# Performance work log

Measured on AMD Instinct MI355X. Metric: run time of the kernel, lower is better.

Reference implementation:

```python
import jax, jax.numpy as jnp
import numpy as np

E, K, H, I, GS, T, C = 64, 4, 2048, 1536, 128, 1024, 128

# FP4 E2M1 lookup table: sign bit in nibble MSB, magnitudes {0,.5,1,1.5,2,3,4,6}
LUT = jnp.array([0.0, 0.5, 1.0, 1.5, 2.0, 3.0, 4.0, 6.0,
                 -0.0, -0.5, -1.0, -1.5, -2.0, -3.0, -4.0, -6.0], dtype=jnp.float32)


def _dequant(packed, scales):
    """packed: [O, I//8] int32 (8 FP4 nibbles/word), scales: [I//GS, O] -> W [O, I] fp32."""
    O, IW = packed.shape
    shifts = (jnp.arange(8, dtype=jnp.int32) * 4)
    nib = (packed[:, :, None] >> shifts) & 0xF          # [O, IW, 8]
    vals = LUT[nib].reshape(O, IW * 8)                   # [O, I]
    g = jnp.arange(IW * 8) // GS                         # group index per input col
    return vals * scales.T[:, g]                         # [O, I]


def _mlp(x2d, gp, gs, up, us, dp, ds):
    """SwiGLU expert: down( silu(x Wg^T) * (x Wu^T) )."""
    Wg = _dequant(gp, gs)
    Wu = _dequant(up, us)
    Wd = _dequant(dp, ds)
    h = jax.nn.silu(x2d @ Wg.T) * (x2d @ Wu.T)           # [N, I]
    return h @ Wd.T                                      # [N, H]


def setup_inputs() -> dict:
    key = jax.random.key(0)
    ks = jax.random.split(key, 16)
    ri = lambda k, sh: jax.random.randint(k, sh, 0, 2**31 - 1, dtype=jnp.int32)
    sc = lambda k, sh: jax.random.uniform(k, sh, dtype=jnp.float32) * 0.02 + 0.001
    return {
        "x": jax.random.normal(ks[0], (T, H), dtype=jnp.float32),
        "gate_w": jax.random.normal(ks[1], (E, H), dtype=jnp.float32) * 0.02,
        "gate_scales": sc(ks[2], (E, H // GS, I)),
        "up_scales": sc(ks[3], (E, H // GS, I)),
        "down_scales": sc(ks[4], (E, I // GS, H)),
        "sh_gate_scales": sc(ks[5], (H // GS, I)),
        "sh_up_scales": sc(ks[6], (H // GS, I)),
        "sh_down_scales": sc(ks[7], (I // GS, H)),
        "gate_packed": ri(ks[8], (E, I, H // 8)),
        "up_packed": ri(ks[9], (E, I, H // 8)),
        "down_packed": ri(ks[10], (E, H, I // 8)),
        "sh_gate_packed": ri(ks[11], (I, H // 8)),
        "sh_up_packed": ri(ks[12], (I, H // 8)),
        "sh_down_packed": ri(ks[13], (H, I // 8)),
    }


def reference(x, gate_w, gate_scales, up_scales, down_scales,
              sh_gate_scales, sh_up_scales, sh_down_scales,
              gate_packed, up_packed, down_packed,
              sh_gate_packed, sh_up_packed, sh_down_packed):
    # --- top-k routing ---
    probs = jax.nn.softmax(x @ gate_w.T, axis=-1)        # [T, E]
    tw, ti = jax.lax.top_k(probs, K)                     # [T, K]
    tw = tw / tw.sum(-1, keepdims=True)
    # --- dispatch with fixed capacity C per expert ---
    A = T * K
    ef = ti.reshape(-1)                                  # [A] expert id per assignment
    tok = jnp.arange(A) // K                             # source token per assignment
    counts = jax.ops.segment_sum(jnp.ones(A, jnp.int32), ef, num_segments=E)
    starts = jnp.cumsum(counts) - counts                 # [E]
    sidx = jnp.argsort(ef)
    pos_sorted = jnp.arange(A, dtype=jnp.int32) - starts[ef[sidx]]
    pos = jnp.zeros(A, jnp.int32).at[sidx].set(pos_sorted)  # rank within expert
    slot = ef * C + pos
    valid = pos < C
    buf = jnp.zeros((E * C + 1, H), x.dtype).at[jnp.where(valid, slot, E * C)].set(x[tok])
    buf = buf[:E * C].reshape(E, C, H)
    # --- per-expert fused dequant + SwiGLU (scan over experts) ---
    def body(_, xs):
        b, gp, gs, up, us, dp, ds = xs
        return None, _mlp(b, gp, gs, up, us, dp, ds)
    _, eout = jax.lax.scan(body, None,
                           (buf, gate_packed, gate_scales, up_packed, up_scales,
                            down_packed, down_scales))
    # --- combine ---
    rows = eout.reshape(E * C, H)
    gath = rows[jnp.where(valid, slot, 0)] * valid[:, None].astype(x.dtype)
    y = (gath.reshape(T, K, H) * tw[..., None]).sum(axis=1)
    # --- shared expert ---
    y = y + _mlp(x, sh_gate_packed, sh_gate_scales, sh_up_packed, sh_up_scales,
                 sh_down_packed, sh_down_scales)
    return y
```

## Files before the change

kernel.cpp:

```cpp
#include <hip/hip_runtime.h>
#include <stdint.h>

#define E_ 64
#define KTOP 4
#define H_ 2048
#define I_ 1536
#define GS_ 128
#define T_ 1024
#define CAP 128

typedef __attribute__((ext_vector_type(8))) short short8;
typedef __attribute__((ext_vector_type(4))) float f32x4;

__device__ __forceinline__ uint32_t bf16rne(float f) {
  uint32_t u = __float_as_uint(f);
  return (u + 0x7FFFu + ((u >> 16) & 1u)) >> 16;
}
__device__ __forceinline__ float bf16f(uint32_t b) {
  return __uint_as_float(b << 16);
}

__global__ void cast_x_kernel(const float* __restrict__ x, uint16_t* __restrict__ xb, int n4) {
  int i = blockIdx.x * blockDim.x + threadIdx.x;
  if (i >= n4) return;
  float4 v = ((const float4*)x)[i];
  uint32_t lo = bf16rne(v.x) | (bf16rne(v.y) << 16);
  uint32_t hi = bf16rne(v.z) | (bf16rne(v.w) << 16);
  uint2 r; r.x = lo; r.y = hi;
  ((uint2*)xb)[i] = r;
}

__global__ void transpose_gw_kernel(const float* __restrict__ gw, float* __restrict__ gwT) {
  int o = blockIdx.x * 256 + threadIdx.x;
  int k = o >> 6, e = o & 63;
  gwT[o] = gw[(long)e * H_ + k];
}

__global__ __launch_bounds__(256) void routing_kernel(
    const float* __restrict__ x, const float* __restrict__ gwT,
    float* __restrict__ tw, int* __restrict__ ti) {
  int t = blockIdx.x;
  int tid = threadIdx.x;
  __shared__ float xs[H_];
  __shared__ float lgp[4][E_];
  const float4* xp = (const float4*)(x + (long)t * H_);
  ((float4*)xs)[tid] = xp[tid];
  ((float4*)xs)[tid + 256] = xp[tid + 256];
  __syncthreads();
  int e = tid & 63, w4 = tid >> 6;
  const float* gp = gwT + (long)w4 * 512 * E_ + e;
  const float* xw = xs + w4 * 512;
  float a0 = 0.f, a1 = 0.f, a2 = 0.f, a3 = 0.f;
#pragma unroll 4
  for (int k = 0; k < 512; k += 4) {
    a0 += xw[k]     * gp[(long)(k)     * E_];
    a1 += xw[k + 1] * gp[(long)(k + 1) * E_];
    a2 += xw[k + 2] * gp[(long)(k + 2) * E_];
    a3 += xw[k + 3] * gp[(long)(k + 3) * E_];
  }
  lgp[w4][e] = (a0 + a1) + (a2 + a3);
  __syncthreads();
  if (tid < 64) {
    int lane = tid;
    float v = lgp[0][lane] + lgp[1][lane] + lgp[2][lane] + lgp[3][lane];
    float vals[KTOP]; int ids[KTOP];
#pragma unroll
    for (int k = 0; k < KTOP; k++) {
      float bv = v; int bi = lane;
      for (int off = 32; off; off >>= 1) {
        float ov = __shfl_xor(bv, off);
        int oi = __shfl_xor(bi, off);
        if (ov > bv || (ov == bv && oi < bi)) { bv = ov; bi = oi; }
      }
      vals[k] = bv; ids[k] = bi;
      if (lane == bi) v = -3.4e38f;
    }
    if (lane == 0) {
      float m = vals[0];
      float p[KTOP]; float s = 0.f;
#pragma unroll
      for (int k = 0; k < KTOP; k++) { p[k] = expf(vals[k] - m); s += p[k]; }
      float inv = 1.f / s;
#pragma unroll
      for (int k = 0; k < KTOP; k++) {
        tw[t * KTOP + k] = p[k] * inv;
        ti[t * KTOP + k] = ids[k];
      }
    }
  }
}

__global__ void assign_kernel(const int* __restrict__ ti, int* __restrict__ counts,
                              int* __restrict__ tlist, int* __restrict__ slot_of) {
  int e = blockIdx.x;
  int lane = threadIdx.x;
  int cnt = 0;
  for (int base = 0; base < T_ * KTOP; base += 64) {
    int a = base + lane;
    int ef = ti[a];
    unsigned long long m = __ballot(ef == e);
    if (ef == e) {
      int rank = cnt + __popcll(m & ((1ull << lane) - 1ull));
      if (rank < CAP) {
        tlist[e * CAP + rank] = a >> 2;
        slot_of[a] = e * CAP + rank;
      } else {
        slot_of[a] = -1;
      }
    }
    cnt += __popcll(m);
  }
  if (lane == 0) counts[e] = min(cnt, CAP);
}

__global__ __launch_bounds__(256, 3) void gemm_fp4_kernel(
    const uint16_t* __restrict__ A1, const uint16_t* __restrict__ A2, int ldA,
    const int* __restrict__ rowids, const int* __restrict__ counts, int nE,
    const int* __restrict__ packed1, long p_stride,
    const float* __restrict__ scales1, long s_stride,
    const int* __restrict__ packed2, const float* __restrict__ scales2,
    void* __restrict__ out1, int of1, void* __restrict__ out2, int of2,
    int K, int N) {
  __shared__ uint16_t As[2][128 * 64];
  __shared__ uint16_t Bs[8 * 128 * 8];

  int yb = blockIdx.y, bn = blockIdx.x;
  int tid = threadIdx.x;
  int wave = tid >> 6, lane = tid & 63;

  const uint16_t* A;
  const int* packed_e;
  const float* scales_e;
  char* outp;
  int of32, row_base, valid;
  const int* rid = nullptr;
  if (yb < nE) {
    int e = yb;
    valid = counts[e];
    if (valid <= 0) return;
    if (valid > 128) valid = 128;
    if (rowids) rid = rowids + e * CAP;
    row_base = e * CAP;
    A = A1;
    packed_e = packed1 + (long)e * p_stride;
    scales_e = scales1 + (long)e * s_stride;
    outp = (char*)out1; of32 = of1;
  } else {
    valid = 128;
    row_base = (yb - nE) * 128;
    A = A2;
    packed_e = packed2;
    scales_e = scales2;
    outp = (char*)out2; of32 = of2;
  }

  const uint16_t* asrc[4];
  int adst[4];
#pragma unroll
  for (int ii = 0; ii < 4; ii++) {
    int inst = wave * 4 + ii;
    int r = inst * 8 + (lane >> 3);
    int rr = r < valid ? r : valid - 1;
    long arow = rid ? (long)rid[rr] : (long)(row_base + rr);
    int g = (lane & 7) ^ (r & 7);
    asrc[ii] = A + arow * (long)ldA + (g << 3);
    adst[ii] = inst * 512;
  }

  int j = tid >> 1, wseg = tid & 1;
  int n_col = bn * 128 + j;
  const int* prow = packed_e + (long)n_col * (K >> 3) + wseg * 4;
  uint16_t* bdst = Bs + ((long)(wseg * 4) * 128 + j) * 8;

  f32x4 acc[4][4];
#pragma unroll
  for (int a0 = 0; a0 < 4; a0++)
#pragma unroll
    for (int b0 = 0; b0 < 4; b0++) {
      f32x4 z = {0.f, 0.f, 0.f, 0.f};
      acc[a0][b0] = z;
    }

  int wm = wave >> 1, wn = wave & 1;
  int q = lane >> 4, r16 = lane & 15;

  int nk = K >> 6;

  uint4 bpk_c = *(const uint4*)prow;
  float scl_c = scales_e[n_col];
#pragma unroll
  for (int ii = 0; ii < 4; ii++)
    __builtin_amdgcn_global_load_lds(
        (const __attribute__((address_space(1))) unsigned int*)asrc[ii],
        (__attribute__((address_space(3))) unsigned int*)(&As[0][0] + adst[ii]),
        16, 0, 0);
  uint4 bpk_n = bpk_c;
  float scl_n = scl_c;

  for (int it = 0; it < nk; ++it) {
    int b = it & 1;
    int kt2 = (it + 1) << 6;
    int pf = (it + 1 < nk);
    if (pf) {
      bpk_n = *(const uint4*)(prow + (kt2 >> 3));
      scl_n = scales_e[(long)(kt2 >> 7) * N + n_col];
      uint16_t* ab = &As[b ^ 1][0];
#pragma unroll
      for (int ii = 0; ii < 4; ii++)
        __builtin_amdgcn_global_load_lds(
            (const __attribute__((address_space(1))) unsigned int*)(asrc[ii] + kt2),
            (__attribute__((address_space(3))) unsigned int*)(ab + adst[ii]),
            16, 0, 0);
    }
    {
      float s = scl_c;
      uint32_t b1 = bf16rne(s), b15 = bf16rne(1.5f * s);
      uint32_t t0 = 0, t1 = b1 - 0x80, t2 = b1, t3 = b15;
      uint32_t t4 = b1 + 0x80, t5 = b15 + 0x80, t6 = b1 + 0x100, t7 = b15 + 0x100;
      uint32_t tll = (t0 & 0xFF) | ((t1 & 0xFF) << 8) | ((t2 & 0xFF) << 16) | ((t3 & 0xFF) << 24);
      uint32_t tlh = (t4 & 0xFF) | ((t5 & 0xFF) << 8) | ((t6 & 0xFF) << 16) | ((t7 & 0xFF) << 24);
      uint32_t thl = (t0 >> 8) | ((t1 >> 8) << 8) | ((t2 >> 8) << 16) | ((t3 >> 8) << 24);
      uint32_t thh = (t4 >> 8) | ((t5 >> 8) << 8) | ((t6 >> 8) << 16) | ((t7 >> 8) << 24);
      uint32_t wsv[4] = {bpk_c.x, bpk_c.y, bpk_c.z, bpk_c.w};
#pragma unroll
      for (int w = 0; w < 4; w++) {
        uint32_t wv = wsv[w];
        uint32_t ev = wv & 0x07070707u;
        uint32_t od = (wv >> 4) & 0x07070707u;
        uint32_t se = (wv << 4) & 0x80808080u;
        uint32_t so = wv & 0x80808080u;
        uint32_t he = __builtin_amdgcn_perm(thh, thl, ev) | se;
        uint32_t ho = __builtin_amdgcn_perm(thh, thl, od) | so;
        uint32_t le = __builtin_amdgcn_perm(tlh, tll, ev);
        uint32_t lo = __builtin_amdgcn_perm(tlh, tll, od);
        uint32_t v02 = __builtin_amdgcn_perm(he, le, 0x05010400u);
        uint32_t v46 = __builtin_amdgcn_perm(he, le, 0x07030602u);
        uint32_t v13 = __builtin_amdgcn_perm(ho, lo, 0x05010400u);
        uint32_t v57 = __builtin_amdgcn_perm(ho, lo, 0x07030602u);
        uint4 qv;
        qv.x = __builtin_amdgcn_perm(v13, v02, 0x05040100u);
        qv.y = __builtin_amdgcn_perm(v13, v02, 0x07060302u);
        qv.z = __builtin_amdgcn_perm(v57, v46, 0x05040100u);
        qv.w = __builtin_amdgcn_perm(v57, v46, 0x07060302u);
        *(uint4*)(bdst + (long)w * 1024) = qv;
      }
    }
    if (pf) asm volatile("s_waitcnt vmcnt(6) lgkmcnt(0)" ::: "memory");
    else    asm volatile("s_waitcnt vmcnt(0) lgkmcnt(0)" ::: "memory");
    __builtin_amdgcn_sched_barrier(0);
    __builtin_amdgcn_s_barrier();
    __builtin_amdgcn_sched_barrier(0);

    const uint16_t* asb = &As[b][0];
    __builtin_amdgcn_s_setprio(1);
#pragma unroll
    for (int kk = 0; kk < 64; kk += 32) {
      int kc4 = (kk >> 3) + q;
      short8 af[4], bfr[4];
#pragma unroll
      for (int fm = 0; fm < 4; fm++) {
        int m = wm * 64 + fm * 16 + r16;
        af[fm] = *(const short8*)(asb + (long)m * 64 + ((kc4 ^ (m & 7)) << 3));
      }
#pragma unroll
      for (int fn = 0; fn < 4; fn++) {
        int n = wn * 64 + fn * 16 + r16;
        bfr[fn] = *(const short8*)(Bs + ((long)kc4 * 128 + n) * 8);
      }
#pragma unroll
      for (int fm = 0; fm < 4; fm++)
#pragma unroll
        for (int fn = 0; fn < 4; fn++)
          acc[fm][fn] = __builtin_amdgcn_mfma_f32_16x16x32_bf16(af[fm], bfr[fn], acc[fm][fn], 0, 0, 0);
    }
    __builtin_amdgcn_s_setprio(0);
    __builtin_amdgcn_sched_barrier(0);
    __builtin_amdgcn_s_barrier();
    __builtin_amdgcn_sched_barrier(0);
    bpk_c = bpk_n;
    scl_c = scl_n;
  }

  int outr0 = wm * 64 + (q << 2);
  int outc0 = bn * 128 + wn * 64 + r16;
#pragma unroll
  for (int fm = 0; fm < 4; fm++)
#pragma unroll
    for (int fn = 0; fn < 4; fn++) {
#pragma unroll
      for (int r = 0; r < 4; r++) {
        int rloc = outr0 + fm * 16 + r;
        if (rloc >= valid) continue;
        long row = row_base + rloc;
        long col = outc0 + fn * 16;
        float vv = acc[fm][fn][r];
        if (of32) ((float*)outp)[row * N + col] = vv;
        else ((uint16_t*)outp)[row * N + col] = (uint16_t)bf16rne(vv);
      }
    }
}

__global__ void silu_mul_kernel(const uint16_t* __restrict__ g, const uint16_t* __restrict__ u,
                                uint16_t* __restrict__ h, int n8) {
  int i = blockIdx.x * blockDim.x + threadIdx.x;
  if (i >= n8) return;
  uint4 gv = ((const uint4*)g)[i];
  uint4 uv = ((const uint4*)u)[i];
  uint32_t gw[4] = {gv.x, gv.y, gv.z, gv.w};
  uint32_t uw[4] = {uv.x, uv.y, uv.z, uv.w};
  uint32_t rw[4];
#pragma unroll
  for (int w = 0; w < 4; w++) {
    float g0 = bf16f(gw[w] & 0xFFFFu), g1 = bf16f(gw[w] >> 16);
    float u0 = bf16f(uw[w] & 0xFFFFu), u1 = bf16f(uw[w] >> 16);
    float r0 = g0 / (1.f + __expf(-g0)) * u0;
    float r1 = g1 / (1.f + __expf(-g1)) * u1;
    rw[w] = bf16rne(r0) | (bf16rne(r1) << 16);
  }
  uint4 res; res.x = rw[0]; res.y = rw[1]; res.z = rw[2]; res.w = rw[3];
  ((uint4*)h)[i] = res;
}

__global__ __launch_bounds__(256) void combine_kernel(
    float* __restrict__ y, const uint16_t* __restrict__ eout,
    const int* __restrict__ slot_of, const float* __restrict__ tw) {
  int t = blockIdx.x;
  int c = threadIdx.x * 8;
  float* yp = y + (long)t * H_ + c;
  float4 y0 = ((float4*)yp)[0];
  float4 y1 = ((float4*)yp)[1];
  float a[8] = {y0.x, y0.y, y0.z, y0.w, y1.x, y1.y, y1.z, y1.w};
#pragma unroll
  for (int k = 0; k < KTOP; k++) {
    int s = slot_of[t * KTOP + k];
    float w = tw[t * KTOP + k];
    if (s < 0) continue;
    uint4 v = *(const uint4*)(eout + (long)s * H_ + c);
    uint32_t vw[4] = {v.x, v.y, v.z, v.w};
#pragma unroll
    for (int jj = 0; jj < 4; jj++) {
      a[2 * jj]     += w * bf16f(vw[jj] & 0xFFFFu);
      a[2 * jj + 1] += w * bf16f(vw[jj] >> 16);
    }
  }
  float4 o0 = {a[0], a[1], a[2], a[3]};
  float4 o1 = {a[4], a[5], a[6], a[7]};
  ((float4*)yp)[0] = o0;
  ((float4*)yp)[1] = o1;
}

extern "C" void kernel_launch(void* const* d_in, const int* in_sizes, int n_in,
                              void* d_out, int out_size, void* d_ws, size_t ws_size,
                              hipStream_t stream) {
  const float* x              = (const float*)d_in[0];
  const float* gate_w         = (const float*)d_in[1];
  const float* gate_scales    = (const float*)d_in[2];
  const float* up_scales      = (const float*)d_in[3];
  const float* down_scales    = (const float*)d_in[4];
  const float* sh_gate_scales = (const float*)d_in[5];
  const float* sh_up_scales   = (const float*)d_in[6];
  const float* sh_down_scales = (const float*)d_in[7];
  const int* gate_packed      = (const int*)d_in[8];
  const int* up_packed        = (const int*)d_in[9];
  const int* down_packed      = (const int*)d_in[10];
  const int* sh_gate_packed   = (const int*)d_in[11];
  const int* sh_up_packed     = (const int*)d_in[12];
  const int* sh_down_packed   = (const int*)d_in[13];
  float* y = (float*)d_out;

  char* ws = (char*)d_ws;
  uint16_t* xb     = (uint16_t*)(ws);
  float*    tw     = (float*)(ws + 4194304);
  int*      ti     = (int*)(ws + 4210688);
  int*      counts = (int*)(ws + 4227072);
  int*      tlist  = (int*)(ws + 4227328);
  int*      slot_of= (int*)(ws + 4260096);
  uint16_t* gbuf   = (uint16_t*)(ws + 4276480);
  float*    gwT    = (float*)(ws + 4276480);
  uint16_t* ubuf   = (uint16_t*)(ws + 29442304);
  uint16_t* eout   = (uint16_t*)(ws + 29442304);
  uint16_t* gsbuf  = (uint16_t*)(ws + 62996736);
  uint16_t* usbuf  = (uint16_t*)(ws + 66142464);

  cast_x_kernel<<<2048, 256, 0, stream>>>(x, xb, T_ * H_ / 4);
  transpose_gw_kernel<<<512, 256, 0, stream>>>(gate_w, gwT);
  routing_kernel<<<T_, 256, 0, stream>>>(x, gwT, tw, ti);
  assign_kernel<<<E_, 64, 0, stream>>>(ti, counts, tlist, slot_of);

  gemm_fp4_kernel<<<dim3(12, 72, 1), 256, 0, stream>>>(
      xb, xb, H_, tlist, counts, E_,
      gate_packed, (long)I_ * (H_ / 8), gate_scales, (long)(H_ / GS_) * I_,
      sh_gate_packed, sh_gate_scales,
      gbuf, 0, gsbuf, 0, H_, I_);
  gemm_fp4_kernel<<<dim3(12, 72, 1), 256, 0, stream>>>(
      xb, xb, H_, tlist, counts, E_,
      up_packed, (long)I_ * (H_ / 8), up_scales, (long)(H_ / GS_) * I_,
      sh_up_packed, sh_up_scales,
      ubuf, 0, usbuf, 0, H_, I_);

  silu_mul_kernel<<<(E_ * CAP * I_ / 8 + 255) / 256, 256, 0, stream>>>(
      gbuf, ubuf, gbuf, E_ * CAP * I_ / 8);
  silu_mul_kernel<<<(T_ * I_ / 8 + 255) / 256, 256, 0, stream>>>(
      gsbuf, usbuf, gsbuf, T_ * I_ / 8);

  gemm_fp4_kernel<<<dim3(16, 72, 1), 256, 0, stream>>>(
      gbuf, gsbuf, I_, nullptr, counts, E_,
      down_packed, (long)H_ * (I_ / 8), down_scales, (long)(I_ / GS_) * H_,
      sh_down_packed, sh_down_scales,
      eout, 0, y, 1, I_, H_);

  combine_kernel<<<T_, 256, 0, stream>>>(y, eout, slot_of, tw);
}
```

Before: 546.1 us.

## Switch to fp16 register-side dequant, merge gate/up GEMMs and fuse small kernels

Activations and intermediates move from bf16 to fp16. FP4 weights are now dequantized straight into MFMA B-fragments in registers with a packed fp16 multiply by the scale, so the LDS B staging buffer and its barrier traffic go away. The x input is pre-permuted so the nibble order lines up, and the gate output columns are permuted back on write. Gate and up GEMMs run in one launch via grid z, the two silu launches are merged, and the cast and transpose kernels are fused into one. The trade-off is fp16 range and precision risk, plus redundant dequant work across the waves that share a column.

```diff
diff --git a/kernel.cpp b/kernel.cpp
--- a/kernel.cpp
+++ b/kernel.cpp
@@ -1,4 +1,5 @@
 #include <hip/hip_runtime.h>
+#include <hip/hip_fp16.h>
 #include <stdint.h>
 
 #define E_ 64
@@ -9,31 +10,57 @@
 #define T_ 1024
 #define CAP 128
 
-typedef __attribute__((ext_vector_type(8))) short short8;
-typedef __attribute__((ext_vector_type(4))) float f32x4;
-
-__device__ __forceinline__ uint32_t bf16rne(float f) {
-  uint32_t u = __float_as_uint(f);
-  return (u + 0x7FFFu + ((u >> 16) & 1u)) >> 16;
-}
-__device__ __forceinline__ float bf16f(uint32_t b) {
-  return __uint_as_float(b << 16);
-}
-
-__global__ void cast_x_kernel(const float* __restrict__ x, uint16_t* __restrict__ xb, int n4) {
-  int i = blockIdx.x * blockDim.x + threadIdx.x;
-  if (i >= n4) return;
-  float4 v = ((const float4*)x)[i];
-  uint32_t lo = bf16rne(v.x) | (bf16rne(v.y) << 16);
-  uint32_t hi = bf16rne(v.z) | (bf16rne(v.w) << 16);
-  uint2 r; r.x = lo; r.y = hi;
-  ((uint2*)xb)[i] = r;
-}
-
-__global__ void transpose_gw_kernel(const float* __restrict__ gw, float* __restrict__ gwT) {
-  int o = blockIdx.x * 256 + threadIdx.x;
-  int k = o >> 6, e = o & 63;
-  gwT[o] = gw[(long)e * H_ + k];
+typedef _Float16 f16x8 __attribute__((ext_vector_type(8)));
+typedef float f32x4 __attribute__((ext_vector_type(4)));
+
+__device__ __forceinline__ uint32_t f16pk(float a, float b) {
+  __half2 h = __floats2half2_rn(a, b);
+  return __builtin_bit_cast(uint32_t, h);
+}
+__device__ __forceinline__ uint32_t h2pk(float s) {
+  uint32_t u = (uint32_t)__builtin_bit_cast(uint16_t, __float2half(s));
+  return u | (u << 16);
+}
+__device__ __forceinline__ uint32_t pkmul(uint32_t a, uint32_t b) {
+  __half2 x = __builtin_bit_cast(__half2, a);
+  __half2 y = __builtin_bit_cast(__half2, b);
+  __half2 r = __hmul2(x, y);
+  return __builtin_bit_cast(uint32_t, r);
+}
+
+__device__ __forceinline__ f16x8 dq_f16(uint32_t w, uint32_t spk) {
+  uint32_t ev = w & 0x07070707u;
+  uint32_t od = (w >> 4) & 0x07070707u;
+  uint32_t se = (w << 4) & 0x80808080u;
+  uint32_t so = w & 0x80808080u;
+  uint32_t he = __builtin_amdgcn_perm(0x46444240u, 0x3E3C3800u, ev) | se;
+  uint32_t ho = __builtin_amdgcn_perm(0x46444240u, 0x3E3C3800u, od) | so;
+  uint4 r;
+  r.x = pkmul(__builtin_amdgcn_perm(he, 0u, 0x05000400u), spk);
+  r.y = pkmul(__builtin_amdgcn_perm(he, 0u, 0x07000600u), spk);
+  r.z = pkmul(__builtin_amdgcn_perm(ho, 0u, 0x05000400u), spk);
+  r.w = pkmul(__builtin_amdgcn_perm(ho, 0u, 0x07000600u), spk);
+  return __builtin_bit_cast(f16x8, r);
+}
+
+__global__ void prep_kernel(const float* __restrict__ x, uint16_t* __restrict__ xb,
+                            const float* __restrict__ gw, float* __restrict__ gwT) {
+  int b = blockIdx.x;
+  if (b < T_ * H_ / 8 / 256) {
+    int i = b * 256 + threadIdx.x;
+    const float4* xp = (const float4*)x;
+    float4 v0 = xp[2 * i], v1 = xp[2 * i + 1];
+    uint4 o;
+    o.x = f16pk(v0.x, v0.z);
+    o.y = f16pk(v1.x, v1.z);
+    o.z = f16pk(v0.y, v0.w);
+    o.w = f16pk(v1.y, v1.w);
+    ((uint4*)xb)[i] = o;
+  } else {
+    int o = (b - T_ * H_ / 8 / 256) * 256 + threadIdx.x;
+    int k = o >> 6, e = o & 63;
+    gwT[o] = gw[(long)e * H_ + k];
+  }
 }
 
 __global__ __launch_bounds__(256) void routing_kernel(
@@ -116,21 +143,22 @@
 __global__ __launch_bounds__(256, 3) void gemm_fp4_kernel(
     const uint16_t* __restrict__ A1, const uint16_t* __restrict__ A2, int ldA,
     const int* __restrict__ rowids, const int* __restrict__ counts, int nE,
-    const int* __restrict__ packed1, long p_stride,
-    const float* __restrict__ scales1, long s_stride,
-    const int* __restrict__ packed2, const float* __restrict__ scales2,
-    void* __restrict__ out1, int of1, void* __restrict__ out2, int of2,
-    int K, int N) {
+    const int* __restrict__ pk_e0, const int* __restrict__ pk_e1,
+    const float* __restrict__ sc_e0, const float* __restrict__ sc_e1,
+    long p_stride, long s_stride,
+    const int* __restrict__ pk_s0, const int* __restrict__ pk_s1,
+    const float* __restrict__ sc_s0, const float* __restrict__ sc_s1,
+    void* __restrict__ out_e0, void* __restrict__ out_e1,
+    void* __restrict__ out_s0, void* __restrict__ out_s1,
+    int K, int N, int of32_e, int of32_s, int perm_out) {
   __shared__ uint16_t As[2][128 * 64];
-  __shared__ uint16_t Bs[8 * 128 * 8];
-
-  int yb = blockIdx.y, bn = blockIdx.x;
-  int tid = threadIdx.x;
-  int wave = tid >> 6, lane = tid & 63;
+
+  int bn = blockIdx.x, yb = blockIdx.y, zs = blockIdx.z;
+  int tid = threadIdx.x, wave = tid >> 6, lane = tid & 63;
 
   const uint16_t* A;
-  const int* packed_e;
-  const float* scales_e;
+  const int* pk;
+  const float* sc;
   char* outp;
   int of32, row_base, valid;
   const int* rid = nullptr;
@@ -142,35 +170,43 @@
     if (rowids) rid = rowids + e * CAP;
     row_base = e * CAP;
     A = A1;
-    packed_e = packed1 + (long)e * p_stride;
-    scales_e = scales1 + (long)e * s_stride;
-    outp = (char*)out1; of32 = of1;
+    pk = (zs ? pk_e1 : pk_e0) + (long)e * p_stride;
+    sc = (zs ? sc_e1 : sc_e0) + (long)e * s_stride;
+    outp = (char*)(zs ? out_e1 : out_e0);
+    of32 = of32_e;
   } else {
     valid = 128;
     row_base = (yb - nE) * 128;
     A = A2;
-    packed_e = packed2;
-    scales_e = scales2;
-    outp = (char*)out2; of32 = of2;
-  }
-
-  const uint16_t* asrc[4];
-  int adst[4];
+    pk = zs ? pk_s1 : pk_s0;
+    sc = zs ? sc_s1 : sc_s0;
+    outp = (char*)(zs ? out_s1 : out_s0);
+    of32 = of32_s;
+  }
+
+  uint32_t a_off[4];
+  int lds_dst[4];
 #pragma unroll
   for (int ii = 0; ii < 4; ii++) {
     int inst = wave * 4 + ii;
     int r = inst * 8 + (lane >> 3);
     int rr = r < valid ? r : valid - 1;
-    long arow = rid ? (long)rid[rr] : (long)(row_base + rr);
-    int g = (lane & 7) ^ (r & 7);
-    asrc[ii] = A + arow * (long)ldA + (g << 3);
-    adst[ii] = inst * 512;
-  }
-
-  int j = tid >> 1, wseg = tid & 1;
-  int n_col = bn * 128 + j;
-  const int* prow = packed_e + (long)n_col * (K >> 3) + wseg * 4;
-  uint16_t* bdst = Bs + ((long)(wseg * 4) * 128 + j) * 8;
+    int arow = rid ? rid[rr] : row_base + rr;
+    a_off[ii] = (uint32_t)arow * (uint32_t)ldA + (uint32_t)((((lane & 7) ^ (r & 7)) << 3));
+    lds_dst[ii] = inst * 512;
+  }
+
+  int wm = wave >> 1, wn = wave & 1;
+  int q = lane >> 4, r16 = lane & 15;
+  int KW = K >> 3;
+
+  uint32_t bw_off[4], sc_off[4];
+#pragma unroll
+  for (int fn = 0; fn < 4; fn++) {
+    int c = bn * 128 + wn * 64 + fn * 16 + r16;
+    bw_off[fn] = (uint32_t)c * (uint32_t)KW + 2 * q;
+    sc_off[fn] = (uint32_t)c;
+  }
 
   f32x4 acc[4][4];
 #pragma unroll
@@ -181,108 +217,70 @@
       acc[a0][b0] = z;
     }
 
-  int wm = wave >> 1, wn = wave & 1;
-  int q = lane >> 4, r16 = lane & 15;
-
   int nk = K >> 6;
 
-  uint4 bpk_c = *(const uint4*)prow;
-  float scl_c = scales_e[n_col];
-#pragma unroll
-  for (int ii = 0; ii < 4; ii++)
-    __builtin_amdgcn_global_load_lds(
-        (const __attribute__((address_space(1))) unsigned int*)asrc[ii],
-        (__attribute__((address_space(3))) unsigned int*)(&As[0][0] + adst[ii]),
-        16, 0, 0);
-  uint4 bpk_n = bpk_c;
-  float scl_n = scl_c;
-
-  for (int it = 0; it < nk; ++it) {
-    int b = it & 1;
-    int kt2 = (it + 1) << 6;
-    int pf = (it + 1 < nk);
-    if (pf) {
-      bpk_n = *(const uint4*)(prow + (kt2 >> 3));
-      scl_n = scales_e[(long)(kt2 >> 7) * N + n_col];
-      uint16_t* ab = &As[b ^ 1][0];
-#pragma unroll
-      for (int ii = 0; ii < 4; ii++)
-        __builtin_amdgcn_global_load_lds(
-            (const __attribute__((address_space(1))) unsigned int*)(asrc[ii] + kt2),
-            (__attribute__((address_space(3))) unsigned int*)(ab + adst[ii]),
-            16, 0, 0);
-    }
-    {
-      float s = scl_c;
-      uint32_t b1 = bf16rne(s), b15 = bf16rne(1.5f * s);
-      uint32_t t0 = 0, t1 = b1 - 0x80, t2 = b1, t3 = b15;
-      uint32_t t4 = b1 + 0x80, t5 = b15 + 0x80, t6 = b1 + 0x100, t7 = b15 + 0x100;
-      uint32_t tll = (t0 & 0xFF) | ((t1 & 0xFF) << 8) | ((t2 & 0xFF) << 16) | ((t3 & 0xFF) << 24);
-      uint32_t tlh = (t4 & 0xFF) | ((t5 & 0xFF) << 8) | ((t6 & 0xFF) << 16) | ((t7 & 0xFF) << 24);
-      uint32_t thl = (t0 >> 8) | ((t1 >> 8) << 8) | ((t2 >> 8) << 16) | ((t3 >> 8) << 24);
-      uint32_t thh = (t4 >> 8) | ((t5 >> 8) << 8) | ((t6 >> 8) << 16) | ((t7 >> 8) << 24);
-      uint32_t wsv[4] = {bpk_c.x, bpk_c.y, bpk_c.z, bpk_c.w};
-#pragma unroll
-      for (int w = 0; w < 4; w++) {
-        uint32_t wv = wsv[w];
-        uint32_t ev = wv & 0x07070707u;
-        uint32_t od = (wv >> 4) & 0x07070707u;
-        uint32_t se = (wv << 4) & 0x80808080u;
-        uint32_t so = wv & 0x80808080u;
-        uint32_t he = __builtin_amdgcn_perm(thh, thl, ev) | se;
-        uint32_t ho = __builtin_amdgcn_perm(thh, thl, od) | so;
-        uint32_t le = __builtin_amdgcn_perm(tlh, tll, ev);
-        uint32_t lo = __builtin_amdgcn_perm(tlh, tll, od);
-        uint32_t v02 = __builtin_amdgcn_perm(he, le, 0x05010400u);
-        uint32_t v46 = __builtin_amdgcn_perm(he, le, 0x07030602u);
-        uint32_t v13 = __builtin_amdgcn_perm(ho, lo, 0x05010400u);
-        uint32_t v57 = __builtin_amdgcn_perm(ho, lo, 0x07030602u);
-        uint4 qv;
-        qv.x = __builtin_amdgcn_perm(v13, v02, 0x05040100u);
-        qv.y = __builtin_amdgcn_perm(v13, v02, 0x07060302u);
-        qv.z = __builtin_amdgcn_perm(v57, v46, 0x05040100u);
-        qv.w = __builtin_amdgcn_perm(v57, v46, 0x07060302u);
-        *(uint4*)(bdst + (long)w * 1024) = qv;
-      }
-    }
-    if (pf) asm volatile("s_waitcnt vmcnt(6) lgkmcnt(0)" ::: "memory");
-    else    asm volatile("s_waitcnt vmcnt(0) lgkmcnt(0)" ::: "memory");
-    __builtin_amdgcn_sched_barrier(0);
-    __builtin_amdgcn_s_barrier();
-    __builtin_amdgcn_sched_barrier(0);
-
-    const uint16_t* asb = &As[b][0];
-    __builtin_amdgcn_s_setprio(1);
-#pragma unroll
-    for (int kk = 0; kk < 64; kk += 32) {
-      int kc4 = (kk >> 3) + q;
-      short8 af[4], bfr[4];
-#pragma unroll
-      for (int fm = 0; fm < 4; fm++) {
-        int m = wm * 64 + fm * 16 + r16;
-        af[fm] = *(const short8*)(asb + (long)m * 64 + ((kc4 ^ (m & 7)) << 3));
-      }
-#pragma unroll
-      for (int fn = 0; fn < 4; fn++) {
-        int n = wn * 64 + fn * 16 + r16;
-        bfr[fn] = *(const short8*)(Bs + ((long)kc4 * 128 + n) * 8);
-      }
-#pragma unroll
-      for (int fm = 0; fm < 4; fm++)
-#pragma unroll
-        for (int fn = 0; fn < 4; fn++)
-          acc[fm][fn] = __builtin_amdgcn_mfma_f32_16x16x32_bf16(af[fm], bfr[fn], acc[fm][fn], 0, 0, 0);
-    }
-    __builtin_amdgcn_s_setprio(0);
-    __builtin_amdgcn_sched_barrier(0);
-    __builtin_amdgcn_s_barrier();
-    __builtin_amdgcn_sched_barrier(0);
-    bpk_c = bpk_n;
-    scl_c = scl_n;
+#define STAGE(BUF, KT) do {                                                     \
+    _Pragma("unroll") for (int ii = 0; ii < 4; ii++)                            \
+      __builtin_amdgcn_global_load_lds(                                         \
+          (const __attribute__((address_space(1))) unsigned int*)(A + (KT) + a_off[ii]), \
+          (__attribute__((address_space(3))) unsigned int*)(&As[BUF][0] + lds_dst[ii]),  \
+          16, 0, 0);                                                            \
+  } while (0)
+
+#define LOADB(BPK, SCL, KT) do {                                                \
+    int ktw = (KT) >> 3;                                                        \
+    int sgb = ((KT) >> 7) * N;                                                  \
+    _Pragma("unroll") for (int fn = 0; fn < 4; fn++) {                          \
+      BPK[fn] = *(const uint2*)(pk + ktw + bw_off[fn]);                         \
+      SCL[fn] = sc[sgb + sc_off[fn]];                                           \
+    }                                                                           \
+  } while (0)
+
+#define SLAB(BUF, S, BPK, SPKA) do {                                            \
+    f16x8 bfr[4], af[4];                                                        \
+    _Pragma("unroll") for (int fn = 0; fn < 4; fn++)                            \
+      bfr[fn] = dq_f16((S) ? BPK[fn].y : BPK[fn].x, SPKA[fn]);                  \
+    _Pragma("unroll") for (int fm = 0; fm < 4; fm++) {                          \
+      int m = wm * 64 + fm * 16 + r16;                                          \
+      int slot = (2 * q + (S)) ^ (m & 7);                                       \
+      af[fm] = *(const f16x8*)(&As[BUF][0] + m * 64 + slot * 8);                \
+    }                                                                           \
+    _Pragma("unroll") for (int fm = 0; fm < 4; fm++)                            \
+      _Pragma("unroll") for (int fn = 0; fn < 4; fn++)                          \
+        acc[fm][fn] = __builtin_amdgcn_mfma_f32_16x16x32_f16(af[fm], bfr[fn], acc[fm][fn], 0, 0, 0); \
+  } while (0)
+
+#define ITER(T, BUF, BPK_C, SCL_C, BPK_N, SCL_N) do {                           \
+    __builtin_amdgcn_sched_barrier(0);                                          \
+    asm volatile("s_waitcnt vmcnt(0)" ::: "memory");                            \
+    __builtin_amdgcn_s_barrier();                                               \
+    __builtin_amdgcn_sched_barrier(0);                                          \
+    if ((T) + 1 < nk) {                                                         \
+      STAGE((BUF) ^ 1, ((T) + 1) << 6);                                         \
+      LOADB(BPK_N, SCL_N, ((T) + 1) << 6);                                      \
+    }                                                                           \
+    uint32_t sp_[4];                                                            \
+    _Pragma("unroll") for (int fn = 0; fn < 4; fn++) sp_[fn] = h2pk(SCL_C[fn]); \
+    __builtin_amdgcn_s_setprio(1);                                              \
+    SLAB(BUF, 0, BPK_C, sp_);                                                   \
+    SLAB(BUF, 1, BPK_C, sp_);                                                   \
+    __builtin_amdgcn_s_setprio(0);                                              \
+  } while (0)
+
+  uint2 bpkA[4], bpkB[4];
+  float sclA[4], sclB[4];
+  STAGE(0, 0);
+  LOADB(bpkA, sclA, 0);
+
+  for (int it = 0; it < nk; it += 2) {
+    ITER(it, 0, bpkA, sclA, bpkB, sclB);
+    ITER(it + 1, 1, bpkB, sclB, bpkA, sclA);
   }
 
   int outr0 = wm * 64 + (q << 2);
   int outc0 = bn * 128 + wn * 64 + r16;
+  int c7 = r16 & 7;
+  int pdel = perm_out ? ((((c7 & 1) << 2) | (c7 >> 1)) - c7) : 0;
 #pragma unroll
   for (int fm = 0; fm < 4; fm++)
 #pragma unroll
@@ -292,33 +290,45 @@
         int rloc = outr0 + fm * 16 + r;
         if (rloc >= valid) continue;
         long row = row_base + rloc;
-        long col = outc0 + fn * 16;
+        long col = outc0 + fn * 16 + pdel;
         float vv = acc[fm][fn][r];
         if (of32) ((float*)outp)[row * N + col] = vv;
-        else ((uint16_t*)outp)[row * N + col] = (uint16_t)bf16rne(vv);
+        else ((uint16_t*)outp)[row * N + col] =
+            __builtin_bit_cast(uint16_t, __float2half(vv));
       }
     }
+#undef STAGE
+#undef LOADB
+#undef SLAB
+#undef ITER
 }
 
 __global__ void silu_mul_kernel(const uint16_t* __restrict__ g, const uint16_t* __restrict__ u,
-                                uint16_t* __restrict__ h, int n8) {
+                                uint16_t* __restrict__ h,
+                                const uint16_t* __restrict__ gs, const uint16_t* __restrict__ us,
+                                uint16_t* __restrict__ hs, int n8e, int n8s) {
   int i = blockIdx.x * blockDim.x + threadIdx.x;
-  if (i >= n8) return;
-  uint4 gv = ((const uint4*)g)[i];
-  uint4 uv = ((const uint4*)u)[i];
+  const uint16_t *G, *U;
+  uint16_t* Hp;
+  int idx;
+  if (i < n8e) { G = g; U = u; Hp = h; idx = i; }
+  else if (i < n8e + n8s) { G = gs; U = us; Hp = hs; idx = i - n8e; }
+  else return;
+  uint4 gv = ((const uint4*)G)[idx];
+  uint4 uv = ((const uint4*)U)[idx];
   uint32_t gw[4] = {gv.x, gv.y, gv.z, gv.w};
   uint32_t uw[4] = {uv.x, uv.y, uv.z, uv.w};
   uint32_t rw[4];
 #pragma unroll
   for (int w = 0; w < 4; w++) {
-    float g0 = bf16f(gw[w] & 0xFFFFu), g1 = bf16f(gw[w] >> 16);
-    float u0 = bf16f(uw[w] & 0xFFFFu), u1 = bf16f(uw[w] >> 16);
-    float r0 = g0 / (1.f + __expf(-g0)) * u0;
-    float r1 = g1 / (1.f + __expf(-g1)) * u1;
-    rw[w] = bf16rne(r0) | (bf16rne(r1) << 16);
+    float2 gf = __half22float2(__builtin_bit_cast(__half2, gw[w]));
+    float2 uf = __half22float2(__builtin_bit_cast(__half2, uw[w]));
+    float r0 = gf.x / (1.f + __expf(-gf.x)) * uf.x;
+    float r1 = gf.y / (1.f + __expf(-gf.y)) * uf.y;
+    rw[w] = f16pk(r0, r1);
   }
   uint4 res; res.x = rw[0]; res.y = rw[1]; res.z = rw[2]; res.w = rw[3];
-  ((uint4*)h)[i] = res;
+  ((uint4*)Hp)[idx] = res;
 }
 
 __global__ __launch_bounds__(256) void combine_kernel(
@@ -339,8 +349,9 @@
     uint32_t vw[4] = {v.x, v.y, v.z, v.w};
 #pragma unroll
     for (int jj = 0; jj < 4; jj++) {
-      a[2 * jj]     += w * bf16f(vw[jj] & 0xFFFFu);
-      a[2 * jj + 1] += w * bf16f(vw[jj] >> 16);
+      float2 f = __half22float2(__builtin_bit_cast(__half2, vw[jj]));
+      a[2 * jj]     += w * f.x;
+      a[2 * jj + 1] += w * f.y;
     }
   }
   float4 o0 = {a[0], a[1], a[2], a[3]};
@@ -382,32 +393,28 @@
   uint16_t* gsbuf  = (uint16_t*)(ws + 62996736);
   uint16_t* usbuf  = (uint16_t*)(ws + 66142464);
 
-  cast_x_kernel<<<2048, 256, 0, stream>>>(x, xb, T_ * H_ / 4);
-  transpose_gw_kernel<<<512, 256, 0, stream>>>(gate_w, gwT);
+  prep_kernel<<<1536, 256, 0, stream>>>(x, xb, gate_w, gwT);
   routing_kernel<<<T_, 256, 0, stream>>>(x, gwT, tw, ti);
   assign_kernel<<<E_, 64, 0, stream>>>(ti, counts, tlist, slot_of);
 
-  gemm_fp4_kernel<<<dim3(12, 72, 1), 256, 0, stream>>>(
+  gemm_fp4_kernel<<<dim3(12, 72, 2), 256, 0, stream>>>(
       xb, xb, H_, tlist, counts, E_,
-      gate_packed, (long)I_ * (H_ / 8), gate_scales, (long)(H_ / GS_) * I_,
-      sh_gate_packed, sh_gate_scales,
-      gbuf, 0, gsbuf, 0, H_, I_);
-  gemm_fp4_kernel<<<dim3(12, 72, 1), 256, 0, stream>>>(
-      xb, xb, H_, tlist, counts, E_,
-      up_packed, (long)I_ * (H_ / 8), up_scales, (long)(H_ / GS_) * I_,
-      sh_up_packed, sh_up_scales,
-      ubuf, 0, usbuf, 0, H_, I_);
-
-  silu_mul_kernel<<<(E_ * CAP * I_ / 8 + 255) / 256, 256, 0, stream>>>(
-      gbuf, ubuf, gbuf, E_ * CAP * I_ / 8);
-  silu_mul_kernel<<<(T_ * I_ / 8 + 255) / 256, 256, 0, stream>>>(
-      gsbuf, usbuf, gsbuf, T_ * I_ / 8);
+      gate_packed, up_packed, gate_scales, up_scales,
+      (long)I_ * (H_ / 8), (long)(H_ / GS_) * I_,
+      sh_gate_packed, sh_up_packed, sh_gate_scales, sh_up_scales,
+      gbuf, ubuf, gsbuf, usbuf,
+      H_, I_, 0, 0, 1);
+
+  silu_mul_kernel<<<(E_ * CAP * I_ / 8 + T_ * I_ / 8) / 256, 256, 0, stream>>>(
+      gbuf, ubuf, gbuf, gsbuf, usbuf, gsbuf, E_ * CAP * I_ / 8, T_ * I_ / 8);
 
   gemm_fp4_kernel<<<dim3(16, 72, 1), 256, 0, stream>>>(
       gbuf, gsbuf, I_, nullptr, counts, E_,
-      down_packed, (long)H_ * (I_ / 8), down_scales, (long)(I_ / GS_) * H_,
-      sh_down_packed, sh_down_scales,
-      eout, 0, y, 1, I_, H_);
+      down_packed, nullptr, down_scales, nullptr,
+      (long)H_ * (I_ / 8), (long)(I_ / GS_) * H_,
+      sh_down_packed, nullptr, sh_down_scales, nullptr,
+      eout, nullptr, y, nullptr,
+      I_, H_, 0, 1, 0);
 
   combine_kernel<<<T_, 256, 0, stream>>>(y, eout, slot_of, tw);
 }
```

Result: slower. 729.7 us (+33.6%).
